# Kernel tuning notes

Measured on AMD Instinct MI355X. Metric: run time of the kernel, lower is better.

The kernel has to match this reference:

```python
import jax, jax.numpy as jnp
import numpy as np

N, E, D, H, C = 50000, 800000, 128, 128, 40
EPS = 1e-5


def setup_inputs() -> dict:
    key = jax.random.key(0)
    ks = jax.random.split(key, 18)
    s = lambda d: 1.0 / np.sqrt(d)
    inp = {
        "x": jax.random.normal(ks[0], (N, D), dtype=jnp.float32),
        "edge_index": jax.random.randint(ks[1], (2, E), 0, N, dtype=jnp.int64),
        # GCNConv weights (x @ W + b after normalized aggregation)
        "W1": jax.random.normal(ks[2], (D, H), dtype=jnp.float32) * s(D),
        "b1": jax.random.normal(ks[3], (H,), dtype=jnp.float32) * 0.01,
        "W2": jax.random.normal(ks[4], (H, H), dtype=jnp.float32) * s(H),
        "b2": jax.random.normal(ks[5], (H,), dtype=jnp.float32) * 0.01,
        "W3": jax.random.normal(ks[6], (H, H), dtype=jnp.float32) * s(H),
        "b3": jax.random.normal(ks[7], (H,), dtype=jnp.float32) * 0.01,
        # LayerNorm params (applied after layers 0 and 1 only)
        "ln1_g": 1.0 + 0.1 * jax.random.normal(ks[8], (H,), dtype=jnp.float32),
        "ln1_b": 0.1 * jax.random.normal(ks[9], (H,), dtype=jnp.float32),
        "ln2_g": 1.0 + 0.1 * jax.random.normal(ks[10], (H,), dtype=jnp.float32),
        "ln2_b": 0.1 * jax.random.normal(ks[11], (H,), dtype=jnp.float32),
        # post_mp MLP head
        "mpW1": jax.random.normal(ks[12], (H, H), dtype=jnp.float32) * s(H),
        "mpb1": jax.random.normal(ks[13], (H,), dtype=jnp.float32) * 0.01,
        "mpW2": jax.random.normal(ks[14], (H, C), dtype=jnp.float32) * s(H),
        "mpb2": jax.random.normal(ks[15], (C,), dtype=jnp.float32) * 0.01,
    }
    return inp


def _layernorm(h, g, b):
    mu = jnp.mean(h, axis=-1, keepdims=True)
    var = jnp.mean((h - mu) ** 2, axis=-1, keepdims=True)
    return (h - mu) * jax.lax.rsqrt(var + EPS) * g + b


def _gcn_forward(x, edge_index, params):
    (W1, b1, W2, b2, W3, b3, ln1_g, ln1_b, ln2_g, ln2_b, mpW1, mpb1, mpW2, mpb2) = params
    n = x.shape[0]
    loop = jnp.arange(n, dtype=edge_index.dtype)
    src = jnp.concatenate([edge_index[0], loop])  # source-to-target flow + self-loops
    dst = jnp.concatenate([edge_index[1], loop])
    deg = jax.ops.segment_sum(jnp.ones_like(src, dtype=x.dtype), dst, num_segments=n)
    dis = jax.lax.rsqrt(deg)  # deg >= 1 due to self-loops
    norm = dis[src] * dis[dst]  # [E+N]

    def conv(h, W, b):
        h = h @ W
        msg = h[src] * norm[:, None]  # gather + scale
        return jax.ops.segment_sum(msg, dst, num_segments=n) + b  # scatter-add

    h = x
    # layer 0
    h = conv(h, W1, b1)
    h = jax.nn.relu(h)  # dropout p=0.1 -> identity in eval
    h = _layernorm(h, ln1_g, ln1_b)
    # layer 1
    h = conv(h, W2, b2)
    h = jax.nn.relu(h)
    h = _layernorm(h, ln2_g, ln2_b)
    # layer 2 (emb is pre-relu conv output)
    emb = conv(h, W3, b3)
    h = jax.nn.relu(emb)
    # post_mp: Linear -> Dropout(eval: identity) -> Linear
    h = h @ mpW1 + mpb1
    logits = h @ mpW2 + mpb2
    return emb, jax.nn.log_softmax(logits, axis=1)


def reference(x, edge_index, W1, b1, W2, b2, W3, b3, ln1_g, ln1_b, ln2_g, ln2_b, mpW1, mpb1, mpW2, mpb2):
    params = (W1, b1, W2, b2, W3, b3, ln1_g, ln1_b, ln2_g, ln2_b, mpW1, mpb1, mpW2, mpb2)
    return _gcn_forward(x, edge_index, params)
```

## Files before the change

kernel.cpp:

```cpp
#include <hip/hip_runtime.h>

typedef __bf16 bf16x8 __attribute__((ext_vector_type(8)));
typedef float  f32x4  __attribute__((ext_vector_type(4)));
typedef float  f32x2  __attribute__((ext_vector_type(2)));
typedef unsigned short u16;
typedef unsigned int   u32;
typedef long long      i64;

#define BSH  7
#define BCAP 4096
#define NPB  256

__device__ __forceinline__ float b2f(u16 x){ return __uint_as_float(((u32)x) << 16); }
__device__ __forceinline__ u16 f2b(float x){
  u32 u = __float_as_uint(x);
  return (u16)((u + 0x7FFFu + ((u >> 16) & 1u)) >> 16);
}

__device__ __forceinline__ void d2acc(u32 pair, f32x2& a){
  f32x2 t;
  t.x = __uint_as_float(pair << 16);
  t.y = __uint_as_float(pair & 0xFFFF0000u);
  a += t;
}
__device__ __forceinline__ void acc8(uint4 q, f32x2* a){
  d2acc(q.x, a[0]); d2acc(q.y, a[1]); d2acc(q.z, a[2]); d2acc(q.w, a[3]);
}

__global__ __launch_bounds__(256) void k_detect(const u16* __restrict__ x,
                                                const u32* __restrict__ ei,
                                                int* __restrict__ flags){
  __shared__ int sh[2];
  int t = threadIdx.x;
  if (t < 2) sh[t] = 0;
  __syncthreads();
  int sane = 0;
  for (int i = t; i < 4096; i += 256){
    u16 u = x[i]; u32 e = (u >> 7) & 0xFFu;
    if (u == 0 || (e >= 0x70u && e <= 0x8Fu)) sane++;
  }
  int nz = 0;
  for (int i = t; i < 1024; i += 256)
    if (ei[2*i + 1] != 0u) nz++;
  atomicAdd(&sh[0], sane);
  atomicAdd(&sh[1], nz);
  __syncthreads();
  if (t == 0){
    flags[0] = (sh[0] < 3500) ? 1 : 0;
    flags[1] = (sh[1] == 0) ? 1 : 0;
  }
}

__device__ __forceinline__ int ld_idx(const void* ei, long long j, int is64){
  return is64 ? (int)((const i64*)ei)[j] : ((const int*)ei)[j];
}
__device__ __forceinline__ void ld8(const void* p, int base, int f, float* o){
  if (f){
    float4 a = *(const float4*)((const float*)p + base);
    float4 b = *(const float4*)((const float*)p + base + 4);
    o[0]=a.x; o[1]=a.y; o[2]=a.z; o[3]=a.w;
    o[4]=b.x; o[5]=b.y; o[6]=b.z; o[7]=b.w;
  } else {
    uint4 q = *(const uint4*)((const u16*)p + base);
    o[0]=b2f((u16)(q.x&0xffff)); o[1]=b2f((u16)(q.x>>16));
    o[2]=b2f((u16)(q.y&0xffff)); o[3]=b2f((u16)(q.y>>16));
    o[4]=b2f((u16)(q.z&0xffff)); o[5]=b2f((u16)(q.z>>16));
    o[6]=b2f((u16)(q.w&0xffff)); o[7]=b2f((u16)(q.w>>16));
  }
}

__global__ __launch_bounds__(256) void k_partA(const void* __restrict__ ei, int E, int n,
                                               int* __restrict__ cntmat,
                                               const int* __restrict__ flags, int nbuk){
  __shared__ int cnt[512];
  int t = threadIdx.x;
  int is64 = flags[1];
  for (int i = t; i < 512; i += 256) cnt[i] = 0;
  __syncthreads();
  long long R = ((long long)E + NPB - 1) / NPB;
  long long lo = (long long)blockIdx.x * R;
  long long hi = lo + R; if (hi > E) hi = E;
  for (long long e = lo + t; e < hi; e += 256){
    int d = ld_idx(ei, (long long)E + e, is64);
    if ((unsigned)d < (unsigned)n) atomicAdd(&cnt[(unsigned)d >> BSH], 1);
  }
  __syncthreads();
  for (int b = t; b < nbuk; b += 256)
    cntmat[(size_t)b*NPB + blockIdx.x] = cnt[b];
}

__global__ __launch_bounds__(NPB) void k_scanBK(const int* __restrict__ cntmat,
                                                int* __restrict__ basemat,
                                                int* __restrict__ bcnt){
  __shared__ int sh[NPB];
  int b = blockIdx.x, t = threadIdx.x;
  int v = cntmat[(size_t)b*NPB + t];
  sh[t] = v; __syncthreads();
  for (int off = 1; off < NPB; off <<= 1){
    int u = 0; if (t >= off) u = sh[t - off];
    __syncthreads(); sh[t] += u; __syncthreads();
  }
  basemat[(size_t)b*NPB + t] = sh[t] - v;
  if (t == NPB-1) bcnt[b] = sh[t];
}

__global__ __launch_bounds__(256) void k_partC(const void* __restrict__ ei, int E, int n,
                                               const int* __restrict__ basemat,
                                               u32* __restrict__ ebuf,
                                               const int* __restrict__ flags, int nbuk){
  __shared__ int cur[512];
  int t = threadIdx.x;
  int is64 = flags[1];
  for (int i = t; i < 512; i += 256) cur[i] = 0;
  __syncthreads();
  for (int b = t; b < nbuk; b += 256) cur[b] = basemat[(size_t)b*NPB + blockIdx.x];
  __syncthreads();
  long long R = ((long long)E + NPB - 1) / NPB;
  long long lo = (long long)blockIdx.x * R;
  long long hi = lo + R; if (hi > E) hi = E;
  for (long long e = lo + t; e < hi; e += 256){
    int d = ld_idx(ei, (long long)E + e, is64);
    int s = ld_idx(ei, e, is64);
    if ((unsigned)d < (unsigned)n && (unsigned)s < (unsigned)n){
      int b = (unsigned)d >> BSH;
      int p = atomicAdd(&cur[b], 1);
      if (p < BCAP) ebuf[(size_t)b*BCAP + p] = (u32)s | ((u32)(d & ((1<<BSH)-1)) << 17);
    }
  }
}

__global__ __launch_bounds__(256) void k_bdeg(const int* __restrict__ bcnt,
                                              const u32* __restrict__ ebuf,
                                              int* __restrict__ deg, int n){
  __shared__ int cnt[1<<BSH];
  int b = blockIdx.x, t = threadIdx.x;
  if (t < (1<<BSH)) cnt[t] = 0;
  __syncthreads();
  int m = bcnt[b]; if (m > BCAP) m = BCAP;
  const u32* eb = ebuf + (size_t)b*BCAP;
  for (int i = t; i < m; i += 256)
    atomicAdd(&cnt[eb[i] >> 17], 1);
  __syncthreads();
  if (t < (1<<BSH)){
    int node = (b << BSH) + t;
    if (node < n) deg[node] = cnt[t];
  }
}

__global__ __launch_bounds__(256) void k_scanA(const int* __restrict__ deg, int n,
                                               int* __restrict__ bsum){
  __shared__ int sh[256];
  int t = threadIdx.x;
  int base = blockIdx.x*1024 + t*4;
  int s = 0;
  #pragma unroll
  for (int i = 0; i < 4; ++i){ int idx = base + i; if (idx < n) s += deg[idx]; }
  sh[t] = s; __syncthreads();
  for (int off = 128; off; off >>= 1){
    if (t < off) sh[t] += sh[t + off];
    __syncthreads();
  }
  if (t == 0) bsum[blockIdx.x] = sh[0];
}

__global__ __launch_bounds__(256) void k_scanB(int* __restrict__ bsum, int nB,
                                               int* __restrict__ rowptr, int n){
  __shared__ int sh[256];
  int t = threadIdx.x;
  int v = (t < nB) ? bsum[t] : 0;
  sh[t] = v; __syncthreads();
  for (int off = 1; off < 256; off <<= 1){
    int u = 0; if (t >= off) u = sh[t - off];
    __syncthreads(); sh[t] += u; __syncthreads();
  }
  if (t < nB) bsum[t] = sh[t] - v;
  if (t == 255) rowptr[n] = sh[255];
}

__global__ __launch_bounds__(256) void k_scanC(const int* __restrict__ deg, int n,
                                               const int* __restrict__ bsum,
                                               int* __restrict__ rowptr,
                                               float* __restrict__ dis){
  __shared__ int sh[256];
  int t = threadIdx.x;
  int base = blockIdx.x*1024 + t*4;
  int d[4]; int s = 0;
  #pragma unroll
  for (int i = 0; i < 4; ++i){ int idx = base + i; d[i] = (idx < n) ? deg[idx] : 0; s += d[i]; }
  sh[t] = s; __syncthreads();
  for (int off = 1; off < 256; off <<= 1){
    int u = 0; if (t >= off) u = sh[t - off];
    __syncthreads(); sh[t] += u; __syncthreads();
  }
  int run = bsum[blockIdx.x] + sh[t] - s;
  #pragma unroll
  for (int i = 0; i < 4; ++i){
    int idx = base + i;
    if (idx < n){
      rowptr[idx] = run; run += d[i];
      dis[idx] = rsqrtf((float)(d[i] + 1));
    }
  }
}

__global__ __launch_bounds__(256) void k_bfill(const int* __restrict__ bcnt,
                                               const u32* __restrict__ ebuf,
                                               const int* __restrict__ rowptr,
                                               int* __restrict__ colx, int n){
  __shared__ int cur[1<<BSH];
  int b = blockIdx.x, t = threadIdx.x;
  if (t < (1<<BSH)){
    int node = (b << BSH) + t;
    cur[t] = (node < n) ? rowptr[node] : 0;
  }
  __syncthreads();
  int m = bcnt[b]; if (m > BCAP) m = BCAP;
  const u32* eb = ebuf + (size_t)b*BCAP;
  for (int i = t; i < m; i += 256){
    u32 e = eb[i];
    int p = atomicAdd(&cur[e >> 17], 1);
    colx[p] = (int)((e & 0x1FFFFu) << 8);
  }
}

__global__ __launch_bounds__(64) void k_shufW(const void* __restrict__ W, u16* __restrict__ Ws,
                                              const int* __restrict__ flags){
  int f = flags[0];
  int bid = blockIdx.x;
  int nt = bid >> 2, kk = bid & 3;
  int l = threadIdx.x;
  int g = l >> 4, mr = l & 15;
  int nn = nt*16 + mr;
  #pragma unroll
  for (int i = 0; i < 8; ++i){
    int k = kk*32 + g*4 + (i & 3) + ((i >> 2) << 4);
    u16 w = f ? f2b(((const float*)W)[k*128 + nn]) : ((const u16*)W)[k*128 + nn];
    Ws[(size_t)(bid*64 + l)*8 + i] = w;
  }
}

__global__ __launch_bounds__(256) void k_gemm(const void* __restrict__ A, int aExt,
    const u16* __restrict__ Ws, const float* __restrict__ dis,
    u16* __restrict__ T, int nTiles, const int* __restrict__ flags)
{
  int wave = threadIdx.x >> 6, lane = threadIdx.x & 63;
  int tile = blockIdx.x*4 + wave;
  if (tile >= nTiles) return;
  int g = lane >> 4, mr = lane & 15;
  int f = aExt ? flags[0] : 0;
  union U8 { ushort4 q[2]; u16 s[8]; bf16x8 b; };
  bf16x8 a[4];
  if (f){
    const float* ap = (const float*)A + (size_t)(tile*16 + mr)*128;
    #pragma unroll
    for (int kk = 0; kk < 4; ++kk){
      float4 p = *(const float4*)(ap + kk*32 + g*4);
      float4 q = *(const float4*)(ap + kk*32 + g*4 + 16);
      U8 u;
      u.s[0]=f2b(p.x); u.s[1]=f2b(p.y); u.s[2]=f2b(p.z); u.s[3]=f2b(p.w);
      u.s[4]=f2b(q.x); u.s[5]=f2b(q.y); u.s[6]=f2b(q.z); u.s[7]=f2b(q.w);
      a[kk] = u.b;
    }
  } else {
    const u16* ap = (const u16*)A + (size_t)(tile*16 + mr)*128;
    #pragma unroll
    for (int kk = 0; kk < 4; ++kk){
      U8 u;
      u.q[0] = *(const ushort4*)(ap + kk*32 + g*4);
      u.q[1] = *(const ushort4*)(ap + kk*32 + g*4 + 16);
      a[kk] = u.b;
    }
  }
  float dj[4];
  #pragma unroll
  for (int j = 0; j < 4; ++j) dj[j] = dis[tile*16 + g*4 + j];
  #pragma unroll
  for (int nt = 0; nt < 8; ++nt){
    f32x4 acc = {0.f,0.f,0.f,0.f};
    #pragma unroll
    for (int kk = 0; kk < 4; ++kk){
      bf16x8 b = *(const bf16x8*)(Ws + (size_t)((nt*4 + kk)*64 + lane)*8);
      acc = __builtin_amdgcn_mfma_f32_16x16x32_bf16(a[kk], b, acc, 0, 0, 0);
    }
    int nn = nt*16 + mr;
    #pragma unroll
    for (int j = 0; j < 4; ++j){
      int row = tile*16 + g*4 + j;
      T[(size_t)row*128 + nn] = f2b(acc[j] * dj[j]);
    }
  }
}

template<int MODE>
__global__ __launch_bounds__(256) void k_agg(const u16* __restrict__ T,
    const int* __restrict__ rowptr, const int* __restrict__ colx,
    const float* __restrict__ dis, const void* __restrict__ bias,
    const void* __restrict__ lg, const void* __restrict__ lb,
    void* __restrict__ outA, int n, const int* __restrict__ flags)
{
  int wave = threadIdx.x >> 6, l = threadIdx.x & 63;
  int v = blockIdx.x*4 + wave; if (v >= n) return;
  int f = flags[0];
  int g = l >> 4, c = l & 15;
  const char* Tb = (const char*)T + c*16;
  f32x2 aA[4] = {};
  f32x2 aB[4] = {};
  if (g == 0){
    uint4 q = *(const uint4*)(Tb + ((size_t)v << 8));
    acc8(q, aA);
  }

  int s = rowptr[v], e = rowptr[v+1];
  int i = s;
  for (; i + 16 <= e; i += 16){
    int o0 = colx[i + g];
    int o1 = colx[i + 4 + g];
    int o2 = colx[i + 8 + g];
    int o3 = colx[i + 12 + g];
    uint4 q0 = *(const uint4*)(Tb + o0);
    uint4 q1 = *(const uint4*)(Tb + o1);
    uint4 q2 = *(const uint4*)(Tb + o2);
    uint4 q3 = *(const uint4*)(Tb + o3);
    acc8(q0, aA); acc8(q1, aB); acc8(q2, aA); acc8(q3, aB);
  }
  for (; i + 4 <= e; i += 4){
    int o = colx[i + g];
    uint4 q = *(const uint4*)(Tb + o);
    acc8(q, aA);
  }
  if (i < e && g < e - i){
    int o = colx[i + g];
    uint4 q = *(const uint4*)(Tb + o);
    acc8(q, aA);
  }

  float acc[8];
  #pragma unroll
  for (int k = 0; k < 4; ++k){
    f32x2 t2 = aA[k] + aB[k];
    float tx = t2.x, ty = t2.y;
    tx += __shfl_xor(tx, 16); tx += __shfl_xor(tx, 32);
    ty += __shfl_xor(ty, 16); ty += __shfl_xor(ty, 32);
    acc[2*k]   = tx;
    acc[2*k+1] = ty;
  }
  float sc = dis[v];
  float bv[8]; ld8(bias, c*8, f, bv);
  float x[8];
  #pragma unroll
  for (int k = 0; k < 8; ++k) x[k] = fmaf(acc[k], sc, bv[k]);

  if (MODE == 0){
    #pragma unroll
    for (int k = 0; k < 8; ++k) x[k] = fmaxf(x[k], 0.f);
    float sum = 0.f;
    #pragma unroll
    for (int k = 0; k < 8; ++k) sum += x[k];
    #pragma unroll
    for (int off = 8; off; off >>= 1) sum += __shfl_xor(sum, off);
    float mu = sum * (1.f/128.f);
    float vs = 0.f;
    #pragma unroll
    for (int k = 0; k < 8; ++k){ float d = x[k] - mu; vs += d*d; }
    #pragma unroll
    for (int off = 8; off; off >>= 1) vs += __shfl_xor(vs, off);
    float inv = rsqrtf(vs*(1.f/128.f) + 1e-5f);
    float gv[8], bvv[8];
    ld8(lg, c*8, f, gv); ld8(lb, c*8, f, bvv);
    if (g == 0){
      uint4 w;
      float y0,y1;
      y0 = (x[0]-mu)*inv*gv[0] + bvv[0]; y1 = (x[1]-mu)*inv*gv[1] + bvv[1];
      w.x = (u32)f2b(y0) | ((u32)f2b(y1) << 16);
      y0 = (x[2]-mu)*inv*gv[2] + bvv[2]; y1 = (x[3]-mu)*inv*gv[3] + bvv[3];
      w.y = (u32)f2b(y0) | ((u32)f2b(y1) << 16);
      y0 = (x[4]-mu)*inv*gv[4] + bvv[4]; y1 = (x[5]-mu)*inv*gv[5] + bvv[5];
      w.z = (u32)f2b(y0) | ((u32)f2b(y1) << 16);
      y0 = (x[6]-mu)*inv*gv[6] + bvv[6]; y1 = (x[7]-mu)*inv*gv[7] + bvv[7];
      w.w = (u32)f2b(y0) | ((u32)f2b(y1) << 16);
      *(uint4*)((u16*)outA + (size_t)v*128 + c*8) = w;
    }
  } else {
    if (g == 0){
      if (f){
        float* oa = (float*)outA + (size_t)v*128 + c*8;
        *(float4*)(oa)     = make_float4(x[0], x[1], x[2], x[3]);
        *(float4*)(oa + 4) = make_float4(x[4], x[5], x[6], x[7]);
      } else {
        uint4 w;
        w.x = (u32)f2b(x[0]) | ((u32)f2b(x[1]) << 16);
        w.y = (u32)f2b(x[2]) | ((u32)f2b(x[3]) << 16);
        w.z = (u32)f2b(x[4]) | ((u32)f2b(x[5]) << 16);
        w.w = (u32)f2b(x[6]) | ((u32)f2b(x[7]) << 16);
        *(uint4*)((u16*)outA + (size_t)v*128 + c*8) = w;
      }
    }
  }
}

__global__ __launch_bounds__(128) void k_wc(const void* __restrict__ mpW1, const void* __restrict__ mpb1,
    const void* __restrict__ mpW2, const void* __restrict__ mpb2,
    float* __restrict__ Wc, float* __restrict__ bc, const int* __restrict__ flags)
{
  int f = flags[0];
  int c = blockIdx.x;
  int k = threadIdx.x;
  float acc = 0.f;
  if (f){
    const float* A  = (const float*)mpW1 + (size_t)k*128;
    const float* B2 = (const float*)mpW2;
    #pragma unroll 8
    for (int j = 0; j < 128; ++j) acc = fmaf(A[j], B2[j*40 + c], acc);
    if (k == 0){
      const float* b1p = (const float*)mpb1;
      float b = ((const float*)mpb2)[c];
      #pragma unroll 8
      for (int j = 0; j < 128; ++j) b = fmaf(b1p[j], B2[j*40 + c], b);
      bc[c] = b;
    }
  } else {
    const u16* A  = (const u16*)mpW1 + (size_t)k*128;
    const u16* B2 = (const u16*)mpW2;
    #pragma unroll 8
    for (int j = 0; j < 128; ++j) acc = fmaf(b2f(A[j]), b2f(B2[j*40 + c]), acc);
    if (k == 0){
      const u16* b1p = (const u16*)mpb1;
      float b = b2f(((const u16*)mpb2)[c]);
      #pragma unroll 8
      for (int j = 0; j < 128; ++j) b = fmaf(b2f(b1p[j]), b2f(B2[j*40 + c]), b);
      bc[c] = b;
    }
  }
  Wc[k*40 + c] = acc;
}

__global__ __launch_bounds__(64) void k_shufWc(const float* __restrict__ Wc, u16* __restrict__ Wcs){
  int bid = blockIdx.x;
  int nt = bid >> 2, kk = bid & 3;
  int l = threadIdx.x;
  int g = l >> 4, mr = l & 15;
  int nn = nt*16 + mr;
  #pragma unroll
  for (int i = 0; i < 8; ++i){
    int k = kk*32 + g*4 + (i & 3) + ((i >> 2) << 4);
    Wcs[(size_t)(bid*64 + l)*8 + i] = (nn < 40) ? f2b(Wc[k*40 + nn]) : (u16)0;
  }
}

__global__ __launch_bounds__(256) void k_logitsM(const u16* __restrict__ Wcs,
    const float* __restrict__ bc, void* __restrict__ dout, int n,
    const int* __restrict__ flags)
{
  int wave = threadIdx.x >> 6, lane = threadIdx.x & 63;
  int tile = blockIdx.x*4 + wave;
  int nTiles = n >> 4;
  if (tile >= nTiles) return;
  int f = flags[0];
  int g = lane >> 4, mr = lane & 15;
  union U8 { ushort4 q[2]; u16 s[8]; bf16x8 b; };
  bf16x8 a[4];
  if (f){
    const float* ap = (const float*)dout + (size_t)(tile*16 + mr)*128;
    #pragma unroll
    for (int kk = 0; kk < 4; ++kk){
      float4 p = *(const float4*)(ap + kk*32 + g*4);
      float4 q = *(const float4*)(ap + kk*32 + g*4 + 16);
      U8 u;
      u.s[0]=f2b(fmaxf(p.x,0.f)); u.s[1]=f2b(fmaxf(p.y,0.f));
      u.s[2]=f2b(fmaxf(p.z,0.f)); u.s[3]=f2b(fmaxf(p.w,0.f));
      u.s[4]=f2b(fmaxf(q.x,0.f)); u.s[5]=f2b(fmaxf(q.y,0.f));
      u.s[6]=f2b(fmaxf(q.z,0.f)); u.s[7]=f2b(fmaxf(q.w,0.f));
      a[kk] = u.b;
    }
  } else {
    const u16* ap = (const u16*)dout + (size_t)(tile*16 + mr)*128;
    #pragma unroll
    for (int kk = 0; kk < 4; ++kk){
      U8 u;
      u.q[0] = *(const ushort4*)(ap + kk*32 + g*4);
      u.q[1] = *(const ushort4*)(ap + kk*32 + g*4 + 16);
      #pragma unroll
      for (int i = 0; i < 8; ++i) u.s[i] = (u.s[i] & 0x8000u) ? (u16)0 : u.s[i];
      a[kk] = u.b;
    }
  }
  f32x4 acc[3];
  #pragma unroll
  for (int nt = 0; nt < 3; ++nt){
    f32x4 c4 = {0.f,0.f,0.f,0.f};
    #pragma unroll
    for (int kk = 0; kk < 4; ++kk){
      bf16x8 b = *(const bf16x8*)(Wcs + (size_t)((nt*4 + kk)*64 + lane)*8);
      c4 = __builtin_amdgcn_mfma_f32_16x16x32_bf16(a[kk], b, c4, 0, 0, 0);
    }
    acc[nt] = c4;
  }
  float bcv[3]; bool valid[3];
  #pragma unroll
  for (int nt = 0; nt < 3; ++nt){
    int c = nt*16 + mr;
    valid[nt] = (c < 40);
    bcv[nt] = valid[nt] ? bc[c] : 0.f;
  }
  float* of = (float*)dout + (size_t)n*128;
  u16*  ob = (u16*) dout + (size_t)n*128;
  #pragma unroll
  for (int j = 0; j < 4; ++j){
    float l0 = valid[0] ? acc[0][j] + bcv[0] : -3.0e38f;
    float l1 = valid[1] ? acc[1][j] + bcv[1] : -3.0e38f;
    float l2 = valid[2] ? acc[2][j] + bcv[2] : -3.0e38f;
    float m = fmaxf(l0, fmaxf(l1, l2));
    #pragma unroll
    for (int off = 8; off; off >>= 1) m = fmaxf(m, __shfl_xor(m, off));
    float ssum = (valid[0] ? expf(l0 - m) : 0.f)
               + (valid[1] ? expf(l1 - m) : 0.f)
               + (valid[2] ? expf(l2 - m) : 0.f);
    #pragma unroll
    for (int off = 8; off; off >>= 1) ssum += __shfl_xor(ssum, off);
    float lgs = m + logf(ssum);
    int node = tile*16 + g*4 + j;
    #pragma unroll
    for (int nt = 0; nt < 3; ++nt){
      if (valid[nt]){
        int c = nt*16 + mr;
        float r = (nt==0 ? l0 : (nt==1 ? l1 : l2)) - lgs;
        if (f) of[(size_t)node*40 + c] = r;
        else   ob[(size_t)node*40 + c] = f2b(r);
      }
    }
  }
}

extern "C" void kernel_launch(void* const* d_in, const int* in_sizes, int n_in,
                              void* d_out, int out_size, void* d_ws, size_t ws_size,
                              hipStream_t stream)
{
  const int n = in_sizes[0] / 128;
  const int E = in_sizes[1] / 2;

  const void* x    = d_in[0];
  const void* ei   = d_in[1];
  const void* W1   = d_in[2];
  const void* b1   = d_in[3];
  const void* W2   = d_in[4];
  const void* b2   = d_in[5];
  const void* W3   = d_in[6];
  const void* b3   = d_in[7];
  const void* ln1g = d_in[8];
  const void* ln1b = d_in[9];
  const void* ln2g = d_in[10];
  const void* ln2b = d_in[11];
  const void* mpW1 = d_in[12];
  const void* mpb1 = d_in[13];
  const void* mpW2 = d_in[14];
  const void* mpb2 = d_in[15];

  u16* Hbuf = (u16*)d_out;

  char* w = (char*)d_ws;
  size_t off = 0;
  auto alloc = [&](size_t bytes)->char*{
    char* p = w + off; off = (off + bytes + 255) & ~(size_t)255; return p;
  };
  const int nbuk = (n + (1<<BSH) - 1) >> BSH;

  int*   flags = (int*)  alloc(256);
  float* dis   = (float*)alloc((size_t)n*4);
  int*   deg   = (int*)  alloc((size_t)n*4);
  int*   rowp  = (int*)  alloc((size_t)(n+1)*4);
  int*   bsum  = (int*)  alloc(1024);
  int*   bcnt  = (int*)  alloc((size_t)nbuk*4);
  int*   cntm  = (int*)  alloc((size_t)nbuk*NPB*4);
  int*   basem = (int*)  alloc((size_t)nbuk*NPB*4);
  u32*   ebuf  = (u32*)  alloc((size_t)nbuk*BCAP*4);
  int*   colx  = (int*)  alloc((size_t)E*4 + 256);
  u16*   T     = (u16*)  alloc((size_t)n*128*2);
  u16*   Ws    = (u16*)  alloc((size_t)128*128*2);
  float* Wc    = (float*)alloc((size_t)128*40*4);
  float* bc    = (float*)alloc((size_t)64*4);
  u16*   Wcs   = (u16*)  alloc((size_t)12*64*8*2);

  int nB = (n + 1023) / 1024;

  k_detect<<<1, 256, 0, stream>>>((const u16*)x, (const u32*)ei, flags);
  k_partA <<<NPB, 256, 0, stream>>>(ei, E, n, cntm, flags, nbuk);
  k_scanBK<<<nbuk, NPB, 0, stream>>>(cntm, basem, bcnt);
  k_partC <<<NPB, 256, 0, stream>>>(ei, E, n, basem, ebuf, flags, nbuk);
  k_bdeg  <<<nbuk, 256, 0, stream>>>(bcnt, ebuf, deg, n);
  k_scanA <<<nB, 256, 0, stream>>>(deg, n, bsum);
  k_scanB <<<1, 256, 0, stream>>>(bsum, nB, rowp, n);
  k_scanC <<<nB, 256, 0, stream>>>(deg, n, bsum, rowp, dis);
  k_bfill <<<nbuk, 256, 0, stream>>>(bcnt, ebuf, rowp, colx, n);
  k_wc    <<<40, 128, 0, stream>>>(mpW1, mpb1, mpW2, mpb2, Wc, bc, flags);
  k_shufWc<<<12, 64, 0, stream>>>(Wc, Wcs);

  int nTiles = (n + 15) / 16;
  int gG = (nTiles + 3) / 4;
  int gA = (n + 3) / 4;

  k_shufW<<<32, 64, 0, stream>>>(W1, Ws, flags);
  k_gemm <<<gG, 256, 0, stream>>>(x, 1, Ws, dis, T, nTiles, flags);
  k_agg<0><<<gA, 256, 0, stream>>>(T, rowp, colx, dis, b1, ln1g, ln1b, Hbuf, n, flags);
  k_shufW<<<32, 64, 0, stream>>>(W2, Ws, flags);
  k_gemm <<<gG, 256, 0, stream>>>(Hbuf, 0, Ws, dis, T, nTiles, flags);
  k_agg<0><<<gA, 256, 0, stream>>>(T, rowp, colx, dis, b2, ln2g, ln2b, Hbuf, n, flags);
  k_shufW<<<32, 64, 0, stream>>>(W3, Ws, flags);
  k_gemm <<<gG, 256, 0, stream>>>(Hbuf, 0, Ws, dis, T, nTiles, flags);
  k_agg<1><<<gA, 256, 0, stream>>>(T, rowp, colx, dis, b3, nullptr, nullptr, d_out, n, flags);
  k_logitsM<<<gG, 256, 0, stream>>>(Wcs, bc, d_out, n, flags);
}
```

Measured before the change: 245.4 us.

## Map one node per 16-lane group in aggregation instead of one per wave

The aggregation kernel now gives each 16-lane quarter-wave its own destination node, so a 256-thread block covers 16 nodes instead of 4. Each group walks its node's whole edge list alone, with four gathers in flight per iteration, which removes the cross-group shuffle reduction and the idle groups on low-degree nodes. In exchange, lanes in one wave can diverge on differing degrees. Out-of-range groups clamp to the last node and skip their store.

```diff
diff --git a/kernel.cpp b/kernel.cpp
--- a/kernel.cpp
+++ b/kernel.cpp
@@ -299,52 +299,44 @@
     void* __restrict__ outA, int n, const int* __restrict__ flags)
 {
   int wave = threadIdx.x >> 6, l = threadIdx.x & 63;
-  int v = blockIdx.x*4 + wave; if (v >= n) return;
+  int g = l >> 4, c = l & 15;
+  int v = blockIdx.x*16 + wave*4 + g;
+  bool alive = v < n;
+  int vv = alive ? v : (n - 1);
   int f = flags[0];
-  int g = l >> 4, c = l & 15;
   const char* Tb = (const char*)T + c*16;
+
   f32x2 aA[4] = {};
   f32x2 aB[4] = {};
-  if (g == 0){
-    uint4 q = *(const uint4*)(Tb + ((size_t)v << 8));
+  {
+    uint4 q = *(const uint4*)(Tb + ((size_t)vv << 8));
     acc8(q, aA);
   }
-
-  int s = rowptr[v], e = rowptr[v+1];
+  int s = rowptr[vv], e = rowptr[vv+1];
   int i = s;
-  for (; i + 16 <= e; i += 16){
-    int o0 = colx[i + g];
-    int o1 = colx[i + 4 + g];
-    int o2 = colx[i + 8 + g];
-    int o3 = colx[i + 12 + g];
+  for (; i + 4 <= e; i += 4){
+    int o0 = colx[i];
+    int o1 = colx[i+1];
+    int o2 = colx[i+2];
+    int o3 = colx[i+3];
     uint4 q0 = *(const uint4*)(Tb + o0);
     uint4 q1 = *(const uint4*)(Tb + o1);
     uint4 q2 = *(const uint4*)(Tb + o2);
     uint4 q3 = *(const uint4*)(Tb + o3);
     acc8(q0, aA); acc8(q1, aB); acc8(q2, aA); acc8(q3, aB);
   }
-  for (; i + 4 <= e; i += 4){
-    int o = colx[i + g];
-    uint4 q = *(const uint4*)(Tb + o);
+  for (; i < e; ++i){
+    uint4 q = *(const uint4*)(Tb + colx[i]);
     acc8(q, aA);
   }
-  if (i < e && g < e - i){
-    int o = colx[i + g];
-    uint4 q = *(const uint4*)(Tb + o);
-    acc8(q, aA);
-  }
 
   float acc[8];
   #pragma unroll
   for (int k = 0; k < 4; ++k){
-    f32x2 t2 = aA[k] + aB[k];
-    float tx = t2.x, ty = t2.y;
-    tx += __shfl_xor(tx, 16); tx += __shfl_xor(tx, 32);
-    ty += __shfl_xor(ty, 16); ty += __shfl_xor(ty, 32);
-    acc[2*k]   = tx;
-    acc[2*k+1] = ty;
-  }
-  float sc = dis[v];
+    acc[2*k]   = aA[k].x + aB[k].x;
+    acc[2*k+1] = aA[k].y + aB[k].y;
+  }
+  float sc = dis[vv];
   float bv[8]; ld8(bias, c*8, f, bv);
   float x[8];
   #pragma unroll
@@ -367,7 +359,7 @@
     float inv = rsqrtf(vs*(1.f/128.f) + 1e-5f);
     float gv[8], bvv[8];
     ld8(lg, c*8, f, gv); ld8(lb, c*8, f, bvv);
-    if (g == 0){
+    if (alive){
       uint4 w;
       float y0,y1;
       y0 = (x[0]-mu)*inv*gv[0] + bvv[0]; y1 = (x[1]-mu)*inv*gv[1] + bvv[1];
@@ -381,7 +373,7 @@
       *(uint4*)((u16*)outA + (size_t)v*128 + c*8) = w;
     }
   } else {
-    if (g == 0){
+    if (alive){
       if (f){
         float* oa = (float*)outA + (size_t)v*128 + c*8;
         *(float4*)(oa)     = make_float4(x[0], x[1], x[2], x[3]);
@@ -596,7 +588,7 @@
 
   int nTiles = (n + 15) / 16;
   int gG = (nTiles + 3) / 4;
-  int gA = (n + 3) / 4;
+  int gA = (n + 15) / 16;
 
   k_shufW<<<32, 64, 0, stream>>>(W1, Ws, flags);
   k_gemm <<<gG, 256, 0, stream>>>(x, 1, Ws, dis, T, nTiles, flags);
```

New measurement: 226.0 us. -7.9%, faster.
